# Performance work log

Measured on AMD Instinct MI355X. Metric: run time of the kernel, lower is better.

## Reference

```python
import jax, jax.numpy as jnp
import numpy as np

EPS = 1e-6  # AngularPhysicsConfig.eps


def setup_inputs() -> dict:
    key = jax.random.key(0)
    k1, k2 = jax.random.split(key)
    B, L, d, H = 2, 2048, 2048, 8
    x_spatial = jax.random.normal(k1, (B, L, d), dtype=jnp.float32)
    # attn is a softmax output: rows sum to 1 over the last axis
    attn = jax.nn.softmax(jax.random.normal(k2, (B, H, L, L), dtype=jnp.float32), axis=-1)
    W = jnp.ones((1,), dtype=jnp.float32)   # nn.Parameter(torch.ones(1))
    b = jnp.zeros((1,), dtype=jnp.float32)  # bias_init = 0.0
    return {"x_spatial": x_spatial, "attn": attn, "W": W, "b": b}


def reference(x_spatial, attn, W, b):
    # --- angular_kernel ---
    norm = jnp.clip(jnp.linalg.norm(x_spatial, axis=-1, keepdims=True), EPS, None)
    x_unit = x_spatial / norm                                   # [B, L, d]
    K = jnp.einsum('bld,bmd->blm', x_unit, x_unit)              # [B, L, L] cosine sim
    K_mean = K.mean(axis=(-1, -2), keepdims=True)
    K_cent = K - K_mean
    # torch .std() is unbiased (ddof=1), computed on detached K_cent
    K_std = jnp.std(jax.lax.stop_gradient(K_cent), axis=(-1, -2), keepdims=True, ddof=1)
    K_norm = K_cent / jnp.clip(K_std, EPS, None)                # [B, L, L]

    # --- compute_cos_align (detach_attn_for_alignment=True) ---
    A = jax.lax.stop_gradient(attn.mean(axis=1))                # [B, L, L]
    cos_align = jnp.sum(A * K_norm, axis=-1)                    # [B, L]

    # --- gate ---
    gate = jax.nn.sigmoid(W * cos_align + b)                    # [B, L]
    return gate, cos_align, K_norm
```

## Files before the change

### kernel.cpp

```cpp
#include <hip/hip_runtime.h>
#include <hip/hip_bf16.h>

#define L_DIM 2048
#define D_DIM 2048
#define B_DIM 2
#define H_DIM 8
#define NT 16
#define NPAIR 136
#define NRED 512
#define NKT (D_DIM / 64)
#define EPSV 1e-6f

using bf16x8 = __attribute__((ext_vector_type(8))) __bf16;
using f32x4  = __attribute__((ext_vector_type(4))) float;
using f4     = __attribute__((ext_vector_type(4))) float;

__device__ inline void gload_lds16(const void* g, void* l) {
    __builtin_amdgcn_global_load_lds(
        (const __attribute__((address_space(1))) void*)g,
        (__attribute__((address_space(3))) void*)l, 16, 0, 0);
}

__device__ inline ushort f2bf(float f) {
    unsigned int u = __float_as_uint(f);
    unsigned int lsb = (u >> 16) & 1u;
    u += 0x7fffu + lsb;
    return (ushort)(u >> 16);
}
__device__ inline float bf2f(ushort u) {
    return __uint_as_float(((unsigned int)u) << 16);
}

__global__ __launch_bounds__(256) void k_normalize(const float* __restrict__ x,
                                                   ushort* __restrict__ xu,
                                                   double* __restrict__ sums) {
    const int row = blockIdx.x;
    const int t   = threadIdx.x;
    const float* xr = x + (size_t)row * D_DIM;
    f4 v0 = __builtin_nontemporal_load(((const f4*)xr) + t);
    f4 v1 = __builtin_nontemporal_load(((const f4*)xr) + t + 256);
    float ss = v0.x*v0.x + v0.y*v0.y + v0.z*v0.z + v0.w*v0.w
             + v1.x*v1.x + v1.y*v1.y + v1.z*v1.z + v1.w*v1.w;
    #pragma unroll
    for (int off = 32; off; off >>= 1) ss += __shfl_down(ss, off);
    __shared__ float red[4];
    __shared__ float s_inv;
    if ((t & 63) == 0) red[t >> 6] = ss;
    __syncthreads();
    if (t == 0) {
        float nrm = sqrtf(red[0] + red[1] + red[2] + red[3]);
        nrm = fmaxf(nrm, EPSV);
        s_inv = 1.0f / nrm;
        if (row == 0) { sums[0] = 0.0; sums[1] = 0.0; sums[2] = 0.0; sums[3] = 0.0; }
    }
    __syncthreads();
    const float inv = s_inv;
    ushort* xo = xu + (size_t)row * D_DIM;
    ushort4 o0, o1;
    o0.x = f2bf(v0.x * inv); o0.y = f2bf(v0.y * inv);
    o0.z = f2bf(v0.z * inv); o0.w = f2bf(v0.w * inv);
    o1.x = f2bf(v1.x * inv); o1.y = f2bf(v1.y * inv);
    o1.z = f2bf(v1.z * inv); o1.w = f2bf(v1.w * inv);
    ((ushort4*)xo)[t]       = o0;
    ((ushort4*)xo)[t + 256] = o1;
}

__global__ __launch_bounds__(256) void k_mixed(const ushort* __restrict__ Xu,
                                               const float* __restrict__ attn,
                                               ushort* __restrict__ K16,
                                               double* __restrict__ sums,
                                               ushort* __restrict__ Amean) {
    __shared__ __align__(16) ushort lds_a[128 * 64];
    __shared__ __align__(16) ushort lds_b[128 * 64];
    const int t = threadIdx.x;
    const int batch = blockIdx.z;

    if (blockIdx.x >= NPAIR) {
        const int rid = blockIdx.x - NPAIR;
        const float* ab = attn + (size_t)batch * H_DIM * L_DIM * L_DIM;
        ushort* am = Amean + (size_t)batch * L_DIM * L_DIM;
        int i = rid * 256 + t;
        #pragma unroll
        for (int j = 0; j < 8; ++j, i += NRED * 256) {
            float4 s = {0.f, 0.f, 0.f, 0.f};
            #pragma unroll
            for (int h = 0; h < H_DIM; ++h) {
                const f4 v = __builtin_nontemporal_load(
                    ((const f4*)(ab + (size_t)h * L_DIM * L_DIM)) + i);
                s.x += v.x; s.y += v.y; s.z += v.z; s.w += v.w;
            }
            ushort4 o;
            o.x = f2bf(s.x * 0.125f); o.y = f2bf(s.y * 0.125f);
            o.z = f2bf(s.z * 0.125f); o.w = f2bf(s.w * 0.125f);
            ((ushort4*)am)[i] = o;
        }
        return;
    }

    const int lane = t & 63;
    const int w    = t >> 6;
    const int wr   = w >> 1, wc = w & 1;
    int ti = 0, rem = blockIdx.x;
    while (rem >= NT - ti) { rem -= NT - ti; ++ti; }
    const int tj = ti + rem;
    const int bRow = ti * 128;
    const int bCol = tj * 128;
    const bool diag = (ti == tj);
    const ushort* Xb = Xu + (size_t)batch * L_DIM * D_DIM;

    const int srow8  = t >> 3;
    const int schunk = ((t & 7) ^ (srow8 & 7)) * 8;
    const ushort* gA = Xb + (size_t)(bRow + srow8) * D_DIM + schunk;
    const ushort* gB = Xb + (size_t)(bCol + srow8) * D_DIM + schunk;
    ushort* lA = lds_a + t * 8;
    ushort* lB = lds_b + t * 8;

    f32x4 acc[4][4] = {};
    const int frow = lane & 15;
    const int fk   = lane >> 4;

    for (int kt = 0; kt < NKT; ++kt) {
        __syncthreads();
        const size_t ko = (size_t)kt * 64;
        #pragma unroll
        for (int i = 0; i < 4; ++i) {
            gload_lds16(gA + ko + (size_t)i * 32 * D_DIM, lA + i * 2048);
            gload_lds16(gB + ko + (size_t)i * 32 * D_DIM, lB + i * 2048);
        }
        __syncthreads();
        #pragma unroll
        for (int ks = 0; ks < 2; ++ks) {
            bf16x8 a[4], b[4];
            #pragma unroll
            for (int m = 0; m < 4; ++m) {
                const int R = wr * 64 + m * 16 + frow;
                a[m] = *(const bf16x8*)&lds_a[R * 64 + (((ks << 2) + fk) ^ (R & 7)) * 8];
            }
            #pragma unroll
            for (int n = 0; n < 4; ++n) {
                const int S = wc * 64 + n * 16 + frow;
                b[n] = *(const bf16x8*)&lds_b[S * 64 + (((ks << 2) + fk) ^ (S & 7)) * 8];
            }
            #pragma unroll
            for (int m = 0; m < 4; ++m)
                #pragma unroll
                for (int n = 0; n < 4; ++n)
                    acc[m][n] = __builtin_amdgcn_mfma_f32_16x16x32_bf16(a[m], b[n], acc[m][n], 0, 0, 0);
        }
    }

    ushort* Kb = K16 + (size_t)batch * L_DIM * L_DIM;
    float ps = 0.f, pss = 0.f;
    #pragma unroll
    for (int m = 0; m < 4; ++m) {
        #pragma unroll
        for (int n = 0; n < 4; ++n) {
            #pragma unroll
            for (int j = 0; j < 4; ++j) {
                const int r = bRow + wr * 64 + m * 16 + fk * 4 + j;
                const int c = bCol + wc * 64 + n * 16 + frow;
                const float v = acc[m][n][j];
                Kb[(size_t)r * L_DIM + c] = f2bf(v);
                ps += v; pss += v * v;
            }
            if (!diag) {
                const int rr  = bCol + wc * 64 + n * 16 + frow;
                const int cc0 = bRow + wr * 64 + m * 16 + fk * 4;
                ushort4 mq;
                mq.x = f2bf(acc[m][n][0]); mq.y = f2bf(acc[m][n][1]);
                mq.z = f2bf(acc[m][n][2]); mq.w = f2bf(acc[m][n][3]);
                *(ushort4*)&Kb[(size_t)rr * L_DIM + cc0] = mq;
            }
        }
    }
    if (!diag) { ps *= 2.f; pss *= 2.f; }
    #pragma unroll
    for (int off = 32; off; off >>= 1) {
        ps  += __shfl_down(ps, off);
        pss += __shfl_down(pss, off);
    }
    __shared__ float redS[4], redSS[4];
    if (lane == 0) { redS[w] = ps; redSS[w] = pss; }
    __syncthreads();
    if (t == 0) {
        atomicAdd(&sums[batch * 2],     (double)(redS[0] + redS[1] + redS[2] + redS[3]));
        atomicAdd(&sums[batch * 2 + 1], (double)(redSS[0] + redSS[1] + redSS[2] + redSS[3]));
    }
}

__global__ __launch_bounds__(256) void k_epilogue(float* __restrict__ out,
                                                  const ushort* __restrict__ K16,
                                                  const ushort* __restrict__ Amean,
                                                  const double* __restrict__ sums,
                                                  const float* __restrict__ Wp,
                                                  const float* __restrict__ bp) {
    const int row = blockIdx.x;
    const int b = row >> 11;
    const int t = threadIdx.x;

    const double N = (double)L_DIM * (double)L_DIM;
    const double mean_d = sums[b * 2] / N;
    double var = (sums[b * 2 + 1] - N * mean_d * mean_d) / (N - 1.0);
    var = var > 0.0 ? var : 0.0;
    float sd = (float)sqrt(var);
    sd = fmaxf(sd, EPSV);
    const float inv_std = 1.0f / sd;
    const float mean = (float)mean_d;

    const ushort* krow = K16 + (size_t)row * L_DIM;
    const ushort* arow = Amean + (size_t)row * L_DIM;
    float* onrm = out + 2 * B_DIM * L_DIM + (size_t)row * L_DIM;

    const ushort4 k0 = ((const ushort4*)krow)[t * 2];
    const ushort4 k1 = ((const ushort4*)krow)[t * 2 + 1];
    const ushort4 a0 = ((const ushort4*)arow)[t * 2];
    const ushort4 a1 = ((const ushort4*)arow)[t * 2 + 1];
    float kf[8] = { bf2f(k0.x), bf2f(k0.y), bf2f(k0.z), bf2f(k0.w),
                    bf2f(k1.x), bf2f(k1.y), bf2f(k1.z), bf2f(k1.w) };
    float af[8] = { bf2f(a0.x), bf2f(a0.y), bf2f(a0.z), bf2f(a0.w),
                    bf2f(a1.x), bf2f(a1.y), bf2f(a1.z), bf2f(a1.w) };
    float dot = 0.f;
    #pragma unroll
    for (int j = 0; j < 8; ++j) dot += af[j] * kf[j];
    f4 n0, n1;
    n0.x = (kf[0] - mean) * inv_std; n0.y = (kf[1] - mean) * inv_std;
    n0.z = (kf[2] - mean) * inv_std; n0.w = (kf[3] - mean) * inv_std;
    n1.x = (kf[4] - mean) * inv_std; n1.y = (kf[5] - mean) * inv_std;
    n1.z = (kf[6] - mean) * inv_std; n1.w = (kf[7] - mean) * inv_std;
    __builtin_nontemporal_store(n0, ((f4*)onrm) + t * 2);
    __builtin_nontemporal_store(n1, ((f4*)onrm) + t * 2 + 1);

    #pragma unroll
    for (int off = 32; off; off >>= 1) dot += __shfl_down(dot, off);
    __shared__ float red[4];
    if ((t & 63) == 0) red[t >> 6] = dot;
    __syncthreads();
    if (t == 0) {
        const float dotv = red[0] + red[1] + red[2] + red[3];
        const float ca = (dotv - mean) * inv_std;
        out[B_DIM * L_DIM + row] = ca;
        const float z = Wp[0] * ca + bp[0];
        out[row] = 1.0f / (1.0f + expf(-z));
    }
}

extern "C" void kernel_launch(void* const* d_in, const int* in_sizes, int n_in,
                              void* d_out, int out_size, void* d_ws, size_t ws_size,
                              hipStream_t stream) {
    const float* x    = (const float*)d_in[0];
    const float* attn = (const float*)d_in[1];
    const float* W    = (const float*)d_in[2];
    const float* bb   = (const float*)d_in[3];
    float* out = (float*)d_out;

    const size_t MAT = (size_t)B_DIM * L_DIM * L_DIM;
    ushort* xu    = (ushort*)d_ws;
    double* sums  = (double*)((char*)d_ws + MAT * 2);
    ushort* Amean = (ushort*)((char*)d_ws + MAT * 2 + 256);
    ushort* K16   = (ushort*)((char*)d_ws + MAT * 4 + 256);

    hipLaunchKernelGGL(k_normalize, dim3(B_DIM * L_DIM), dim3(256), 0, stream,
                       x, xu, sums);
    hipLaunchKernelGGL(k_mixed, dim3(NPAIR + NRED, 1, B_DIM), dim3(256), 0, stream,
                       xu, attn, K16, sums, Amean);
    hipLaunchKernelGGL(k_epilogue, dim3(B_DIM * L_DIM), dim3(256), 0, stream,
                       out, K16, Amean, sums, W, bb);
}
```

Measured before the change: 106.1 us.

## Fuse three kernels into one persistent cooperative kernel with grid syncs

Replaces the normalize, mixed GEMM/attn-mean, and epilogue kernels with a single cooperative persistent kernel of 512 blocks. Phase one normalizes rows and starts the attention head-mean. After a grid sync, 272 blocks run the Gram GEMM tiles while the remaining blocks finish the attention reduction. A second grid sync precedes the normalized-output epilogue. This removes two kernel launches and overlaps the GEMM with bandwidth-bound attention reads, at the cost of grid-sync overhead and fixed work partitioning with fewer blocks per phase.

```diff
diff --git a/kernel.cpp b/kernel.cpp
--- a/kernel.cpp
+++ b/kernel.cpp
@@ -1,5 +1,8 @@
 #include <hip/hip_runtime.h>
 #include <hip/hip_bf16.h>
+#include <hip/hip_cooperative_groups.h>
+
+namespace cg = cooperative_groups;
 
 #define L_DIM 2048
 #define D_DIM 2048
@@ -8,6 +11,10 @@
 #define NT 16
 #define NPAIR 136
 #define NRED 512
+#define NUNIT 8192
+#define P1U 6144
+#define NBLK 512
+#define ROWS_PB 8
 #define NKT (D_DIM / 64)
 #define EPSV 1e-6f
 
@@ -31,216 +38,239 @@
     return __uint_as_float(((unsigned int)u) << 16);
 }
 
-__global__ __launch_bounds__(256) void k_normalize(const float* __restrict__ x,
-                                                   ushort* __restrict__ xu,
-                                                   double* __restrict__ sums) {
-    const int row = blockIdx.x;
-    const int t   = threadIdx.x;
-    const float* xr = x + (size_t)row * D_DIM;
-    f4 v0 = __builtin_nontemporal_load(((const f4*)xr) + t);
-    f4 v1 = __builtin_nontemporal_load(((const f4*)xr) + t + 256);
-    float ss = v0.x*v0.x + v0.y*v0.y + v0.z*v0.z + v0.w*v0.w
-             + v1.x*v1.x + v1.y*v1.y + v1.z*v1.z + v1.w*v1.w;
+__device__ __forceinline__ void attn_unit(const float* __restrict__ attn,
+                                          ushort* __restrict__ Amean,
+                                          int u, int t) {
+    const int batch = u >> 12;
+    const int v     = u & 4095;
+    const int rid   = v & (NRED - 1);
+    const int j     = v >> 9;
+    const int i     = rid * 256 + j * (NRED * 256) + t;
+    const float* ab = attn + (size_t)batch * H_DIM * L_DIM * L_DIM;
+    float4 s = {0.f, 0.f, 0.f, 0.f};
     #pragma unroll
-    for (int off = 32; off; off >>= 1) ss += __shfl_down(ss, off);
-    __shared__ float red[4];
-    __shared__ float s_inv;
-    if ((t & 63) == 0) red[t >> 6] = ss;
-    __syncthreads();
-    if (t == 0) {
-        float nrm = sqrtf(red[0] + red[1] + red[2] + red[3]);
-        nrm = fmaxf(nrm, EPSV);
-        s_inv = 1.0f / nrm;
-        if (row == 0) { sums[0] = 0.0; sums[1] = 0.0; sums[2] = 0.0; sums[3] = 0.0; }
-    }
-    __syncthreads();
-    const float inv = s_inv;
-    ushort* xo = xu + (size_t)row * D_DIM;
-    ushort4 o0, o1;
-    o0.x = f2bf(v0.x * inv); o0.y = f2bf(v0.y * inv);
-    o0.z = f2bf(v0.z * inv); o0.w = f2bf(v0.w * inv);
-    o1.x = f2bf(v1.x * inv); o1.y = f2bf(v1.y * inv);
-    o1.z = f2bf(v1.z * inv); o1.w = f2bf(v1.w * inv);
-    ((ushort4*)xo)[t]       = o0;
-    ((ushort4*)xo)[t + 256] = o1;
-}
-
-__global__ __launch_bounds__(256) void k_mixed(const ushort* __restrict__ Xu,
-                                               const float* __restrict__ attn,
-                                               ushort* __restrict__ K16,
-                                               double* __restrict__ sums,
-                                               ushort* __restrict__ Amean) {
+    for (int h = 0; h < H_DIM; ++h) {
+        const f4 vv = __builtin_nontemporal_load(
+            ((const f4*)(ab + (size_t)h * L_DIM * L_DIM)) + i);
+        s.x += vv.x; s.y += vv.y; s.z += vv.z; s.w += vv.w;
+    }
+    ushort4 o;
+    o.x = f2bf(s.x * 0.125f); o.y = f2bf(s.y * 0.125f);
+    o.z = f2bf(s.z * 0.125f); o.w = f2bf(s.w * 0.125f);
+    ((ushort4*)(Amean + (size_t)batch * L_DIM * L_DIM))[i] = o;
+}
+
+__global__ __launch_bounds__(256, 2) void k_fused(const float* __restrict__ x,
+                                                  const float* __restrict__ attn,
+                                                  float* __restrict__ out,
+                                                  ushort* __restrict__ xu,
+                                                  ushort* __restrict__ K16,
+                                                  ushort* __restrict__ Amean,
+                                                  double* __restrict__ sums,
+                                                  const float* __restrict__ Wp,
+                                                  const float* __restrict__ bp) {
     __shared__ __align__(16) ushort lds_a[128 * 64];
     __shared__ __align__(16) ushort lds_b[128 * 64];
-    const int t = threadIdx.x;
-    const int batch = blockIdx.z;
-
-    if (blockIdx.x >= NPAIR) {
-        const int rid = blockIdx.x - NPAIR;
-        const float* ab = attn + (size_t)batch * H_DIM * L_DIM * L_DIM;
-        ushort* am = Amean + (size_t)batch * L_DIM * L_DIM;
-        int i = rid * 256 + t;
-        #pragma unroll
-        for (int j = 0; j < 8; ++j, i += NRED * 256) {
-            float4 s = {0.f, 0.f, 0.f, 0.f};
+    __shared__ float red[4];
+    __shared__ float sbc;
+    const int t   = threadIdx.x;
+    const int blk = blockIdx.x;
+    cg::grid_group grid = cg::this_grid();
+
+    if (blk == 0 && t < 4) sums[t] = 0.0;
+
+    for (int r = 0; r < ROWS_PB; ++r) {
+        const int row = blk * ROWS_PB + r;
+        const float* xr = x + (size_t)row * D_DIM;
+        f4 v0 = __builtin_nontemporal_load(((const f4*)xr) + t);
+        f4 v1 = __builtin_nontemporal_load(((const f4*)xr) + t + 256);
+        float ss = v0.x*v0.x + v0.y*v0.y + v0.z*v0.z + v0.w*v0.w
+                 + v1.x*v1.x + v1.y*v1.y + v1.z*v1.z + v1.w*v1.w;
+        #pragma unroll
+        for (int off = 32; off; off >>= 1) ss += __shfl_down(ss, off);
+        if ((t & 63) == 0) red[t >> 6] = ss;
+        __syncthreads();
+        if (t == 0) {
+            float nrm = sqrtf(red[0] + red[1] + red[2] + red[3]);
+            sbc = 1.0f / fmaxf(nrm, EPSV);
+        }
+        __syncthreads();
+        const float inv = sbc;
+        ushort* xo = xu + (size_t)row * D_DIM;
+        ushort4 o0, o1;
+        o0.x = f2bf(v0.x * inv); o0.y = f2bf(v0.y * inv);
+        o0.z = f2bf(v0.z * inv); o0.w = f2bf(v0.w * inv);
+        o1.x = f2bf(v1.x * inv); o1.y = f2bf(v1.y * inv);
+        o1.z = f2bf(v1.z * inv); o1.w = f2bf(v1.w * inv);
+        ((ushort4*)xo)[t]       = o0;
+        ((ushort4*)xo)[t + 256] = o1;
+        __syncthreads();
+    }
+    #pragma unroll 2
+    for (int k = 0; k < P1U / NBLK; ++k)
+        attn_unit(attn, Amean, blk * (P1U / NBLK) + k, t);
+
+    __threadfence();
+    grid.sync();
+
+    if (blk < 2 * NPAIR) {
+        const int lane = t & 63;
+        const int w    = t >> 6;
+        const int wr   = w >> 1, wc = w & 1;
+        const int batch = blk / NPAIR;
+        int ti = 0, rem = blk % NPAIR;
+        while (rem >= NT - ti) { rem -= NT - ti; ++ti; }
+        const int tj = ti + rem;
+        const int bRow = ti * 128;
+        const int bCol = tj * 128;
+        const bool diag = (ti == tj);
+        const ushort* Xb = xu + (size_t)batch * L_DIM * D_DIM;
+
+        const int srow8  = t >> 3;
+        const int schunk = ((t & 7) ^ (srow8 & 7)) * 8;
+        const ushort* gA = Xb + (size_t)(bRow + srow8) * D_DIM + schunk;
+        const ushort* gB = Xb + (size_t)(bCol + srow8) * D_DIM + schunk;
+        ushort* lA = lds_a + t * 8;
+        ushort* lB = lds_b + t * 8;
+
+        f32x4 acc[4][4] = {};
+        const int frow = lane & 15;
+        const int fk   = lane >> 4;
+
+        for (int kt = 0; kt < NKT; ++kt) {
+            __syncthreads();
+            const size_t ko = (size_t)kt * 64;
             #pragma unroll
-            for (int h = 0; h < H_DIM; ++h) {
-                const f4 v = __builtin_nontemporal_load(
-                    ((const f4*)(ab + (size_t)h * L_DIM * L_DIM)) + i);
-                s.x += v.x; s.y += v.y; s.z += v.z; s.w += v.w;
+            for (int i = 0; i < 4; ++i) {
+                gload_lds16(gA + ko + (size_t)i * 32 * D_DIM, lA + i * 2048);
+                gload_lds16(gB + ko + (size_t)i * 32 * D_DIM, lB + i * 2048);
             }
-            ushort4 o;
-            o.x = f2bf(s.x * 0.125f); o.y = f2bf(s.y * 0.125f);
-            o.z = f2bf(s.z * 0.125f); o.w = f2bf(s.w * 0.125f);
-            ((ushort4*)am)[i] = o;
-        }
-        return;
-    }
-
-    const int lane = t & 63;
-    const int w    = t >> 6;
-    const int wr   = w >> 1, wc = w & 1;
-    int ti = 0, rem = blockIdx.x;
-    while (rem >= NT - ti) { rem -= NT - ti; ++ti; }
-    const int tj = ti + rem;
-    const int bRow = ti * 128;
-    const int bCol = tj * 128;
-    const bool diag = (ti == tj);
-    const ushort* Xb = Xu + (size_t)batch * L_DIM * D_DIM;
-
-    const int srow8  = t >> 3;
-    const int schunk = ((t & 7) ^ (srow8 & 7)) * 8;
-    const ushort* gA = Xb + (size_t)(bRow + srow8) * D_DIM + schunk;
-    const ushort* gB = Xb + (size_t)(bCol + srow8) * D_DIM + schunk;
-    ushort* lA = lds_a + t * 8;
-    ushort* lB = lds_b + t * 8;
-
-    f32x4 acc[4][4] = {};
-    const int frow = lane & 15;
-    const int fk   = lane >> 4;
-
-    for (int kt = 0; kt < NKT; ++kt) {
-        __syncthreads();
-        const size_t ko = (size_t)kt * 64;
-        #pragma unroll
-        for (int i = 0; i < 4; ++i) {
-            gload_lds16(gA + ko + (size_t)i * 32 * D_DIM, lA + i * 2048);
-            gload_lds16(gB + ko + (size_t)i * 32 * D_DIM, lB + i * 2048);
-        }
-        __syncthreads();
-        #pragma unroll
-        for (int ks = 0; ks < 2; ++ks) {
-            bf16x8 a[4], b[4];
+            __syncthreads();
             #pragma unroll
-            for (int m = 0; m < 4; ++m) {
-                const int R = wr * 64 + m * 16 + frow;
-                a[m] = *(const bf16x8*)&lds_a[R * 64 + (((ks << 2) + fk) ^ (R & 7)) * 8];
+            for (int ks = 0; ks < 2; ++ks) {
+                bf16x8 a[4], b[4];
+                #pragma unroll
+                for (int m = 0; m < 4; ++m) {
+                    const int R = wr * 64 + m * 16 + frow;
+                    a[m] = *(const bf16x8*)&lds_a[R * 64 + (((ks << 2) + fk) ^ (R & 7)) * 8];
+                }
+                #pragma unroll
+                for (int n = 0; n < 4; ++n) {
+                    const int S = wc * 64 + n * 16 + frow;
+                    b[n] = *(const bf16x8*)&lds_b[S * 64 + (((ks << 2) + fk) ^ (S & 7)) * 8];
+                }
+                #pragma unroll
+                for (int m = 0; m < 4; ++m)
+                    #pragma unroll
+                    for (int n = 0; n < 4; ++n)
+                        acc[m][n] = __builtin_amdgcn_mfma_f32_16x16x32_bf16(a[m], b[n], acc[m][n], 0, 0, 0);
             }
+        }
+
+        ushort* Kb = K16 + (size_t)batch * L_DIM * L_DIM;
+        float ps = 0.f, pss = 0.f;
+        #pragma unroll
+        for (int m = 0; m < 4; ++m) {
             #pragma unroll
             for (int n = 0; n < 4; ++n) {
-                const int S = wc * 64 + n * 16 + frow;
-                b[n] = *(const bf16x8*)&lds_b[S * 64 + (((ks << 2) + fk) ^ (S & 7)) * 8];
+                #pragma unroll
+                for (int j = 0; j < 4; ++j) {
+                    const int r = bRow + wr * 64 + m * 16 + fk * 4 + j;
+                    const int c = bCol + wc * 64 + n * 16 + frow;
+                    const float v = acc[m][n][j];
+                    Kb[(size_t)r * L_DIM + c] = f2bf(v);
+                    ps += v; pss += v * v;
+                }
+                if (!diag) {
+                    const int rr  = bCol + wc * 64 + n * 16 + frow;
+                    const int cc0 = bRow + wr * 64 + m * 16 + fk * 4;
+                    ushort4 mq;
+                    mq.x = f2bf(acc[m][n][0]); mq.y = f2bf(acc[m][n][1]);
+                    mq.z = f2bf(acc[m][n][2]); mq.w = f2bf(acc[m][n][3]);
+                    *(ushort4*)&Kb[(size_t)rr * L_DIM + cc0] = mq;
+                }
             }
-            #pragma unroll
-            for (int m = 0; m < 4; ++m)
-                #pragma unroll
-                for (int n = 0; n < 4; ++n)
-                    acc[m][n] = __builtin_amdgcn_mfma_f32_16x16x32_bf16(a[m], b[n], acc[m][n], 0, 0, 0);
-        }
-    }
-
-    ushort* Kb = K16 + (size_t)batch * L_DIM * L_DIM;
-    float ps = 0.f, pss = 0.f;
+        }
+        if (!diag) { ps *= 2.f; pss *= 2.f; }
+        #pragma unroll
+        for (int off = 32; off; off >>= 1) {
+            ps  += __shfl_down(ps, off);
+            pss += __shfl_down(pss, off);
+        }
+        __syncthreads();
+        if (lane == 0) red[w] = ps;
+        __syncthreads();
+        const float psum = red[0] + red[1] + red[2] + red[3];
+        __syncthreads();
+        if (lane == 0) red[w] = pss;
+        __syncthreads();
+        if (t == 0) {
+            atomicAdd(&sums[batch * 2],     (double)psum);
+            atomicAdd(&sums[batch * 2 + 1], (double)(red[0] + red[1] + red[2] + red[3]));
+        }
+    } else {
+        const int i0 = blk - 2 * NPAIR;
+        #pragma unroll 2
+        for (int k = 0; k < 9; ++k) {
+            const int u = P1U + i0 + 240 * k;
+            if (u < NUNIT) attn_unit(attn, Amean, u, t);
+        }
+    }
+
+    __threadfence();
+    grid.sync();
+
+    const double N = (double)L_DIM * (double)L_DIM;
+    float mean_b[2], inv_b[2];
     #pragma unroll
-    for (int m = 0; m < 4; ++m) {
-        #pragma unroll
-        for (int n = 0; n < 4; ++n) {
-            #pragma unroll
-            for (int j = 0; j < 4; ++j) {
-                const int r = bRow + wr * 64 + m * 16 + fk * 4 + j;
-                const int c = bCol + wc * 64 + n * 16 + frow;
-                const float v = acc[m][n][j];
-                Kb[(size_t)r * L_DIM + c] = f2bf(v);
-                ps += v; pss += v * v;
-            }
-            if (!diag) {
-                const int rr  = bCol + wc * 64 + n * 16 + frow;
-                const int cc0 = bRow + wr * 64 + m * 16 + fk * 4;
-                ushort4 mq;
-                mq.x = f2bf(acc[m][n][0]); mq.y = f2bf(acc[m][n][1]);
-                mq.z = f2bf(acc[m][n][2]); mq.w = f2bf(acc[m][n][3]);
-                *(ushort4*)&Kb[(size_t)rr * L_DIM + cc0] = mq;
-            }
-        }
-    }
-    if (!diag) { ps *= 2.f; pss *= 2.f; }
-    #pragma unroll
-    for (int off = 32; off; off >>= 1) {
-        ps  += __shfl_down(ps, off);
-        pss += __shfl_down(pss, off);
-    }
-    __shared__ float redS[4], redSS[4];
-    if (lane == 0) { redS[w] = ps; redSS[w] = pss; }
-    __syncthreads();
-    if (t == 0) {
-        atomicAdd(&sums[batch * 2],     (double)(redS[0] + redS[1] + redS[2] + redS[3]));
-        atomicAdd(&sums[batch * 2 + 1], (double)(redSS[0] + redSS[1] + redSS[2] + redSS[3]));
-    }
-}
-
-__global__ __launch_bounds__(256) void k_epilogue(float* __restrict__ out,
-                                                  const ushort* __restrict__ K16,
-                                                  const ushort* __restrict__ Amean,
-                                                  const double* __restrict__ sums,
-                                                  const float* __restrict__ Wp,
-                                                  const float* __restrict__ bp) {
-    const int row = blockIdx.x;
-    const int b = row >> 11;
-    const int t = threadIdx.x;
-
-    const double N = (double)L_DIM * (double)L_DIM;
-    const double mean_d = sums[b * 2] / N;
-    double var = (sums[b * 2 + 1] - N * mean_d * mean_d) / (N - 1.0);
-    var = var > 0.0 ? var : 0.0;
-    float sd = (float)sqrt(var);
-    sd = fmaxf(sd, EPSV);
-    const float inv_std = 1.0f / sd;
-    const float mean = (float)mean_d;
-
-    const ushort* krow = K16 + (size_t)row * L_DIM;
-    const ushort* arow = Amean + (size_t)row * L_DIM;
-    float* onrm = out + 2 * B_DIM * L_DIM + (size_t)row * L_DIM;
-
-    const ushort4 k0 = ((const ushort4*)krow)[t * 2];
-    const ushort4 k1 = ((const ushort4*)krow)[t * 2 + 1];
-    const ushort4 a0 = ((const ushort4*)arow)[t * 2];
-    const ushort4 a1 = ((const ushort4*)arow)[t * 2 + 1];
-    float kf[8] = { bf2f(k0.x), bf2f(k0.y), bf2f(k0.z), bf2f(k0.w),
-                    bf2f(k1.x), bf2f(k1.y), bf2f(k1.z), bf2f(k1.w) };
-    float af[8] = { bf2f(a0.x), bf2f(a0.y), bf2f(a0.z), bf2f(a0.w),
-                    bf2f(a1.x), bf2f(a1.y), bf2f(a1.z), bf2f(a1.w) };
-    float dot = 0.f;
-    #pragma unroll
-    for (int j = 0; j < 8; ++j) dot += af[j] * kf[j];
-    f4 n0, n1;
-    n0.x = (kf[0] - mean) * inv_std; n0.y = (kf[1] - mean) * inv_std;
-    n0.z = (kf[2] - mean) * inv_std; n0.w = (kf[3] - mean) * inv_std;
-    n1.x = (kf[4] - mean) * inv_std; n1.y = (kf[5] - mean) * inv_std;
-    n1.z = (kf[6] - mean) * inv_std; n1.w = (kf[7] - mean) * inv_std;
-    __builtin_nontemporal_store(n0, ((f4*)onrm) + t * 2);
-    __builtin_nontemporal_store(n1, ((f4*)onrm) + t * 2 + 1);
-
-    #pragma unroll
-    for (int off = 32; off; off >>= 1) dot += __shfl_down(dot, off);
-    __shared__ float red[4];
-    if ((t & 63) == 0) red[t >> 6] = dot;
-    __syncthreads();
-    if (t == 0) {
-        const float dotv = red[0] + red[1] + red[2] + red[3];
-        const float ca = (dotv - mean) * inv_std;
-        out[B_DIM * L_DIM + row] = ca;
-        const float z = Wp[0] * ca + bp[0];
-        out[row] = 1.0f / (1.0f + expf(-z));
+    for (int bb = 0; bb < 2; ++bb) {
+        const double mean_d = sums[bb * 2] / N;
+        double var = (sums[bb * 2 + 1] - N * mean_d * mean_d) / (N - 1.0);
+        var = var > 0.0 ? var : 0.0;
+        float sd = fmaxf((float)sqrt(var), EPSV);
+        mean_b[bb] = (float)mean_d;
+        inv_b[bb]  = 1.0f / sd;
+    }
+    const float Wv = Wp[0], bv = bp[0];
+
+    for (int r = 0; r < ROWS_PB; ++r) {
+        const int row = blk * ROWS_PB + r;
+        const int b = row >> 11;
+        const float mean = mean_b[b], inv_std = inv_b[b];
+        const ushort* krow = K16 + (size_t)row * L_DIM;
+        const ushort* arow = Amean + (size_t)row * L_DIM;
+        float* onrm = out + 2 * B_DIM * L_DIM + (size_t)row * L_DIM;
+
+        const ushort4 k0 = ((const ushort4*)krow)[t * 2];
+        const ushort4 k1 = ((const ushort4*)krow)[t * 2 + 1];
+        const ushort4 a0 = ((const ushort4*)arow)[t * 2];
+        const ushort4 a1 = ((const ushort4*)arow)[t * 2 + 1];
+        float kf[8] = { bf2f(k0.x), bf2f(k0.y), bf2f(k0.z), bf2f(k0.w),
+                        bf2f(k1.x), bf2f(k1.y), bf2f(k1.z), bf2f(k1.w) };
+        float af[8] = { bf2f(a0.x), bf2f(a0.y), bf2f(a0.z), bf2f(a0.w),
+                        bf2f(a1.x), bf2f(a1.y), bf2f(a1.z), bf2f(a1.w) };
+        float dot = 0.f;
+        #pragma unroll
+        for (int j = 0; j < 8; ++j) dot += af[j] * kf[j];
+        f4 n0, n1;
+        n0.x = (kf[0] - mean) * inv_std; n0.y = (kf[1] - mean) * inv_std;
+        n0.z = (kf[2] - mean) * inv_std; n0.w = (kf[3] - mean) * inv_std;
+        n1.x = (kf[4] - mean) * inv_std; n1.y = (kf[5] - mean) * inv_std;
+        n1.z = (kf[6] - mean) * inv_std; n1.w = (kf[7] - mean) * inv_std;
+        __builtin_nontemporal_store(n0, ((f4*)onrm) + t * 2);
+        __builtin_nontemporal_store(n1, ((f4*)onrm) + t * 2 + 1);
+
+        #pragma unroll
+        for (int off = 32; off; off >>= 1) dot += __shfl_down(dot, off);
+        if ((t & 63) == 0) red[t >> 6] = dot;
+        __syncthreads();
+        if (t == 0) {
+            const float dotv = red[0] + red[1] + red[2] + red[3];
+            const float ca = (dotv - mean) * inv_std;
+            out[B_DIM * L_DIM + row] = ca;
+            out[row] = 1.0f / (1.0f + expf(-(Wv * ca + bv)));
+        }
+        __syncthreads();
     }
 }
 
@@ -259,10 +289,7 @@
     ushort* Amean = (ushort*)((char*)d_ws + MAT * 2 + 256);
     ushort* K16   = (ushort*)((char*)d_ws + MAT * 4 + 256);
 
-    hipLaunchKernelGGL(k_normalize, dim3(B_DIM * L_DIM), dim3(256), 0, stream,
-                       x, xu, sums);
-    hipLaunchKernelGGL(k_mixed, dim3(NPAIR + NRED, 1, B_DIM), dim3(256), 0, stream,
-                       xu, attn, K16, sums, Amean);
-    hipLaunchKernelGGL(k_epilogue, dim3(B_DIM * L_DIM), dim3(256), 0, stream,
-                       out, K16, Amean, sums, W, bb);
-}
+    void* args[] = { (void*)&x, (void*)&attn, (void*)&out, (void*)&xu,
+                     (void*)&K16, (void*)&Amean, (void*)&sums, (void*)&W, (void*)&bb };
+    hipLaunchCooperativeKernel((void*)k_fused, dim3(NBLK), dim3(256), args, 0, stream);
+}
```

Result: slower. 403.3 us (+280.1%).

## Dynamically schedule attention-mean work via atomic counter across all blocks

Applied to the files above, without the earlier changes.

Replaces the static split, where dedicated blocks each reduced eight fixed attention chunks, with a work queue driven by a global atomic counter. Every block, including the GEMM tile blocks once their tile is done, pulls pairs of attention-mean units until the 8192 units are consumed. This is meant to balance the memory-bound head reduction against the compute-bound Gram tiles so neither side leaves CUs idle. It adds atomic contention, two extra barriers per grab, and a counter reset in the normalize kernel.

```diff
diff --git a/kernel.cpp b/kernel.cpp
--- a/kernel.cpp
+++ b/kernel.cpp
@@ -8,6 +8,8 @@
 #define NT 16
 #define NPAIR 136
 #define NRED 512
+#define NUNIT 8192
+#define NSTREAM 512
 #define NKT (D_DIM / 64)
 #define EPSV 1e-6f
 
@@ -31,9 +33,32 @@
     return __uint_as_float(((unsigned int)u) << 16);
 }
 
+__device__ __forceinline__ void attn_unit(const float* __restrict__ attn,
+                                          ushort* __restrict__ Amean,
+                                          int u, int t) {
+    const int batch = u >> 12;
+    const int v     = u & 4095;
+    const int rid   = v & (NRED - 1);
+    const int j     = v >> 9;
+    const int i     = rid * 256 + j * (NRED * 256) + t;
+    const float* ab = attn + (size_t)batch * H_DIM * L_DIM * L_DIM;
+    float4 s = {0.f, 0.f, 0.f, 0.f};
+    #pragma unroll
+    for (int h = 0; h < H_DIM; ++h) {
+        const f4 vv = __builtin_nontemporal_load(
+            ((const f4*)(ab + (size_t)h * L_DIM * L_DIM)) + i);
+        s.x += vv.x; s.y += vv.y; s.z += vv.z; s.w += vv.w;
+    }
+    ushort4 o;
+    o.x = f2bf(s.x * 0.125f); o.y = f2bf(s.y * 0.125f);
+    o.z = f2bf(s.z * 0.125f); o.w = f2bf(s.w * 0.125f);
+    ((ushort4*)(Amean + (size_t)batch * L_DIM * L_DIM))[i] = o;
+}
+
 __global__ __launch_bounds__(256) void k_normalize(const float* __restrict__ x,
                                                    ushort* __restrict__ xu,
-                                                   double* __restrict__ sums) {
+                                                   double* __restrict__ sums,
+                                                   unsigned int* __restrict__ ctr) {
     const int row = blockIdx.x;
     const int t   = threadIdx.x;
     const float* xr = x + (size_t)row * D_DIM;
@@ -51,7 +76,10 @@
         float nrm = sqrtf(red[0] + red[1] + red[2] + red[3]);
         nrm = fmaxf(nrm, EPSV);
         s_inv = 1.0f / nrm;
-        if (row == 0) { sums[0] = 0.0; sums[1] = 0.0; sums[2] = 0.0; sums[3] = 0.0; }
+        if (row == 0) {
+            sums[0] = 0.0; sums[1] = 0.0; sums[2] = 0.0; sums[3] = 0.0;
+            ctr[0] = 0u;
+        }
     }
     __syncthreads();
     const float inv = s_inv;
@@ -69,122 +97,114 @@
                                                const float* __restrict__ attn,
                                                ushort* __restrict__ K16,
                                                double* __restrict__ sums,
-                                               ushort* __restrict__ Amean) {
+                                               ushort* __restrict__ Amean,
+                                               unsigned int* __restrict__ ctr) {
     __shared__ __align__(16) ushort lds_a[128 * 64];
     __shared__ __align__(16) ushort lds_b[128 * 64];
+    __shared__ unsigned int su;
     const int t = threadIdx.x;
     const int batch = blockIdx.z;
 
-    if (blockIdx.x >= NPAIR) {
-        const int rid = blockIdx.x - NPAIR;
-        const float* ab = attn + (size_t)batch * H_DIM * L_DIM * L_DIM;
-        ushort* am = Amean + (size_t)batch * L_DIM * L_DIM;
-        int i = rid * 256 + t;
+    if (blockIdx.x < NPAIR) {
+        const int lane = t & 63;
+        const int w    = t >> 6;
+        const int wr   = w >> 1, wc = w & 1;
+        int ti = 0, rem = blockIdx.x;
+        while (rem >= NT - ti) { rem -= NT - ti; ++ti; }
+        const int tj = ti + rem;
+        const int bRow = ti * 128;
+        const int bCol = tj * 128;
+        const bool diag = (ti == tj);
+        const ushort* Xb = Xu + (size_t)batch * L_DIM * D_DIM;
+
+        const int srow8  = t >> 3;
+        const int schunk = ((t & 7) ^ (srow8 & 7)) * 8;
+        const ushort* gA = Xb + (size_t)(bRow + srow8) * D_DIM + schunk;
+        const ushort* gB = Xb + (size_t)(bCol + srow8) * D_DIM + schunk;
+        ushort* lA = lds_a + t * 8;
+        ushort* lB = lds_b + t * 8;
+
+        f32x4 acc[4][4] = {};
+        const int frow = lane & 15;
+        const int fk   = lane >> 4;
+
+        for (int kt = 0; kt < NKT; ++kt) {
+            __syncthreads();
+            const size_t ko = (size_t)kt * 64;
+            #pragma unroll
+            for (int i = 0; i < 4; ++i) {
+                gload_lds16(gA + ko + (size_t)i * 32 * D_DIM, lA + i * 2048);
+                gload_lds16(gB + ko + (size_t)i * 32 * D_DIM, lB + i * 2048);
+            }
+            __syncthreads();
+            #pragma unroll
+            for (int ks = 0; ks < 2; ++ks) {
+                bf16x8 a[4], b[4];
+                #pragma unroll
+                for (int m = 0; m < 4; ++m) {
+                    const int R = wr * 64 + m * 16 + frow;
+                    a[m] = *(const bf16x8*)&lds_a[R * 64 + (((ks << 2) + fk) ^ (R & 7)) * 8];
+                }
+                #pragma unroll
+                for (int n = 0; n < 4; ++n) {
+                    const int S = wc * 64 + n * 16 + frow;
+                    b[n] = *(const bf16x8*)&lds_b[S * 64 + (((ks << 2) + fk) ^ (S & 7)) * 8];
+                }
+                #pragma unroll
+                for (int m = 0; m < 4; ++m)
+                    #pragma unroll
+                    for (int n = 0; n < 4; ++n)
+                        acc[m][n] = __builtin_amdgcn_mfma_f32_16x16x32_bf16(a[m], b[n], acc[m][n], 0, 0, 0);
+            }
+        }
+
+        ushort* Kb = K16 + (size_t)batch * L_DIM * L_DIM;
+        float ps = 0.f, pss = 0.f;
         #pragma unroll
-        for (int j = 0; j < 8; ++j, i += NRED * 256) {
-            float4 s = {0.f, 0.f, 0.f, 0.f};
-            #pragma unroll
-            for (int h = 0; h < H_DIM; ++h) {
-                const f4 v = __builtin_nontemporal_load(
-                    ((const f4*)(ab + (size_t)h * L_DIM * L_DIM)) + i);
-                s.x += v.x; s.y += v.y; s.z += v.z; s.w += v.w;
-            }
-            ushort4 o;
-            o.x = f2bf(s.x * 0.125f); o.y = f2bf(s.y * 0.125f);
-            o.z = f2bf(s.z * 0.125f); o.w = f2bf(s.w * 0.125f);
-            ((ushort4*)am)[i] = o;
-        }
-        return;
-    }
-
-    const int lane = t & 63;
-    const int w    = t >> 6;
-    const int wr   = w >> 1, wc = w & 1;
-    int ti = 0, rem = blockIdx.x;
-    while (rem >= NT - ti) { rem -= NT - ti; ++ti; }
-    const int tj = ti + rem;
-    const int bRow = ti * 128;
-    const int bCol = tj * 128;
-    const bool diag = (ti == tj);
-    const ushort* Xb = Xu + (size_t)batch * L_DIM * D_DIM;
-
-    const int srow8  = t >> 3;
-    const int schunk = ((t & 7) ^ (srow8 & 7)) * 8;
-    const ushort* gA = Xb + (size_t)(bRow + srow8) * D_DIM + schunk;
-    const ushort* gB = Xb + (size_t)(bCol + srow8) * D_DIM + schunk;
-    ushort* lA = lds_a + t * 8;
-    ushort* lB = lds_b + t * 8;
-
-    f32x4 acc[4][4] = {};
-    const int frow = lane & 15;
-    const int fk   = lane >> 4;
-
-    for (int kt = 0; kt < NKT; ++kt) {
-        __syncthreads();
-        const size_t ko = (size_t)kt * 64;
-        #pragma unroll
-        for (int i = 0; i < 4; ++i) {
-            gload_lds16(gA + ko + (size_t)i * 32 * D_DIM, lA + i * 2048);
-            gload_lds16(gB + ko + (size_t)i * 32 * D_DIM, lB + i * 2048);
-        }
-        __syncthreads();
-        #pragma unroll
-        for (int ks = 0; ks < 2; ++ks) {
-            bf16x8 a[4], b[4];
-            #pragma unroll
-            for (int m = 0; m < 4; ++m) {
-                const int R = wr * 64 + m * 16 + frow;
-                a[m] = *(const bf16x8*)&lds_a[R * 64 + (((ks << 2) + fk) ^ (R & 7)) * 8];
-            }
+        for (int m = 0; m < 4; ++m) {
             #pragma unroll
             for (int n = 0; n < 4; ++n) {
-                const int S = wc * 64 + n * 16 + frow;
-                b[n] = *(const bf16x8*)&lds_b[S * 64 + (((ks << 2) + fk) ^ (S & 7)) * 8];
+                #pragma unroll
+                for (int j = 0; j < 4; ++j) {
+                    const int r = bRow + wr * 64 + m * 16 + fk * 4 + j;
+                    const int c = bCol + wc * 64 + n * 16 + frow;
+                    const float v = acc[m][n][j];
+                    Kb[(size_t)r * L_DIM + c] = f2bf(v);
+                    ps += v; pss += v * v;
+                }
+                if (!diag) {
+                    const int rr  = bCol + wc * 64 + n * 16 + frow;
+                    const int cc0 = bRow + wr * 64 + m * 16 + fk * 4;
+                    ushort4 mq;
+                    mq.x = f2bf(acc[m][n][0]); mq.y = f2bf(acc[m][n][1]);
+                    mq.z = f2bf(acc[m][n][2]); mq.w = f2bf(acc[m][n][3]);
+                    *(ushort4*)&Kb[(size_t)rr * L_DIM + cc0] = mq;
+                }
             }
-            #pragma unroll
-            for (int m = 0; m < 4; ++m)
-                #pragma unroll
-                for (int n = 0; n < 4; ++n)
-                    acc[m][n] = __builtin_amdgcn_mfma_f32_16x16x32_bf16(a[m], b[n], acc[m][n], 0, 0, 0);
-        }
-    }
-
-    ushort* Kb = K16 + (size_t)batch * L_DIM * L_DIM;
-    float ps = 0.f, pss = 0.f;
-    #pragma unroll
-    for (int m = 0; m < 4; ++m) {
+        }
+        if (!diag) { ps *= 2.f; pss *= 2.f; }
         #pragma unroll
-        for (int n = 0; n < 4; ++n) {
-            #pragma unroll
-            for (int j = 0; j < 4; ++j) {
-                const int r = bRow + wr * 64 + m * 16 + fk * 4 + j;
-                const int c = bCol + wc * 64 + n * 16 + frow;
-                const float v = acc[m][n][j];
-                Kb[(size_t)r * L_DIM + c] = f2bf(v);
-                ps += v; pss += v * v;
-            }
-            if (!diag) {
-                const int rr  = bCol + wc * 64 + n * 16 + frow;
-                const int cc0 = bRow + wr * 64 + m * 16 + fk * 4;
-                ushort4 mq;
-                mq.x = f2bf(acc[m][n][0]); mq.y = f2bf(acc[m][n][1]);
-                mq.z = f2bf(acc[m][n][2]); mq.w = f2bf(acc[m][n][3]);
-                *(ushort4*)&Kb[(size_t)rr * L_DIM + cc0] = mq;
-            }
-        }
-    }
-    if (!diag) { ps *= 2.f; pss *= 2.f; }
-    #pragma unroll
-    for (int off = 32; off; off >>= 1) {
-        ps  += __shfl_down(ps, off);
-        pss += __shfl_down(pss, off);
-    }
-    __shared__ float redS[4], redSS[4];
-    if (lane == 0) { redS[w] = ps; redSS[w] = pss; }
-    __syncthreads();
-    if (t == 0) {
-        atomicAdd(&sums[batch * 2],     (double)(redS[0] + redS[1] + redS[2] + redS[3]));
-        atomicAdd(&sums[batch * 2 + 1], (double)(redSS[0] + redSS[1] + redSS[2] + redSS[3]));
+        for (int off = 32; off; off >>= 1) {
+            ps  += __shfl_down(ps, off);
+            pss += __shfl_down(pss, off);
+        }
+        __shared__ float redS[4], redSS[4];
+        if (lane == 0) { redS[w] = ps; redSS[w] = pss; }
+        __syncthreads();
+        if (t == 0) {
+            atomicAdd(&sums[batch * 2],     (double)(redS[0] + redS[1] + redS[2] + redS[3]));
+            atomicAdd(&sums[batch * 2 + 1], (double)(redSS[0] + redSS[1] + redSS[2] + redSS[3]));
+        }
+    }
+
+    for (;;) {
+        if (t == 0) su = atomicAdd(ctr, 2u);
+        __syncthreads();
+        const unsigned int u = su;
+        __syncthreads();
+        if (u >= NUNIT) break;
+        attn_unit(attn, Amean, (int)u, t);
+        if (u + 1 < NUNIT) attn_unit(attn, Amean, (int)(u + 1), t);
     }
 }
 
@@ -256,13 +276,14 @@
     const size_t MAT = (size_t)B_DIM * L_DIM * L_DIM;
     ushort* xu    = (ushort*)d_ws;
     double* sums  = (double*)((char*)d_ws + MAT * 2);
+    unsigned int* ctr = (unsigned int*)((char*)d_ws + MAT * 2 + 64);
     ushort* Amean = (ushort*)((char*)d_ws + MAT * 2 + 256);
     ushort* K16   = (ushort*)((char*)d_ws + MAT * 4 + 256);
 
     hipLaunchKernelGGL(k_normalize, dim3(B_DIM * L_DIM), dim3(256), 0, stream,
-                       x, xu, sums);
-    hipLaunchKernelGGL(k_mixed, dim3(NPAIR + NRED, 1, B_DIM), dim3(256), 0, stream,
-                       xu, attn, K16, sums, Amean);
+                       x, xu, sums, ctr);
+    hipLaunchKernelGGL(k_mixed, dim3(NPAIR + NSTREAM, 1, B_DIM), dim3(256), 0, stream,
+                       xu, attn, K16, sums, Amean, ctr);
     hipLaunchKernelGGL(k_epilogue, dim3(B_DIM * L_DIM), dim3(256), 0, stream,
                        out, K16, Amean, sums, W, bb);
 }
```

Result: slower. 141.1 us (+33.0%).

## Fuse normalize into mixed kernel with flag-based producer/consumer sync

Applied to the files above, without the earlier changes.

Folds the row-normalization kernel into the mixed kernel. Normalize blocks process 8 rows each, then signal per-tile flags with release atomics, and GEMM blocks spin-wait on the flags for their two row tiles. Normalize blocks then take a share of the attention-mean streaming work, and the remaining attention blocks run unconditionally. This removes one kernel launch boundary and lets the bandwidth-bound attention reduction overlap with normalization and GEMM, at the cost of a memset, spin-waiting that depends on block scheduling order, and a risk of deadlock if GEMM blocks occupy the slots the normalize blocks need.

```diff
diff --git a/kernel.cpp b/kernel.cpp
--- a/kernel.cpp
+++ b/kernel.cpp
@@ -8,6 +8,9 @@
 #define NT 16
 #define NPAIR 136
 #define NRED 512
+#define NNORM 512
+#define NSTR 768
+#define NGEMM (2 * NPAIR)
 #define NKT (D_DIM / 64)
 #define EPSV 1e-6f
 
@@ -31,82 +34,111 @@
     return __uint_as_float(((unsigned int)u) << 16);
 }
 
-__global__ __launch_bounds__(256) void k_normalize(const float* __restrict__ x,
-                                                   ushort* __restrict__ xu,
-                                                   double* __restrict__ sums) {
-    const int row = blockIdx.x;
-    const int t   = threadIdx.x;
-    const float* xr = x + (size_t)row * D_DIM;
-    f4 v0 = __builtin_nontemporal_load(((const f4*)xr) + t);
-    f4 v1 = __builtin_nontemporal_load(((const f4*)xr) + t + 256);
-    float ss = v0.x*v0.x + v0.y*v0.y + v0.z*v0.z + v0.w*v0.w
-             + v1.x*v1.x + v1.y*v1.y + v1.z*v1.z + v1.w*v1.w;
-    #pragma unroll
-    for (int off = 32; off; off >>= 1) ss += __shfl_down(ss, off);
+__device__ __forceinline__ void attn_unit(const float* __restrict__ attn,
+                                          ushort* __restrict__ Amean,
+                                          int job, int j, int t) {
+    const int batch = job >> 9;
+    const int rid   = job & (NRED - 1);
+    const int i     = rid * 256 + j * (NRED * 256) + t;
+    const float* ab = attn + (size_t)batch * H_DIM * L_DIM * L_DIM;
+    float4 s = {0.f, 0.f, 0.f, 0.f};
+    #pragma unroll
+    for (int h = 0; h < H_DIM; ++h) {
+        const f4 vv = __builtin_nontemporal_load(
+            ((const f4*)(ab + (size_t)h * L_DIM * L_DIM)) + i);
+        s.x += vv.x; s.y += vv.y; s.z += vv.z; s.w += vv.w;
+    }
+    ushort4 o;
+    o.x = f2bf(s.x * 0.125f); o.y = f2bf(s.y * 0.125f);
+    o.z = f2bf(s.z * 0.125f); o.w = f2bf(s.w * 0.125f);
+    ((ushort4*)(Amean + (size_t)batch * L_DIM * L_DIM))[i] = o;
+}
+
+__global__ __launch_bounds__(256) void k_mixed(const float* __restrict__ x,
+                                               const float* __restrict__ attn,
+                                               ushort* __restrict__ xu,
+                                               ushort* __restrict__ K16,
+                                               double* __restrict__ sums,
+                                               ushort* __restrict__ Amean,
+                                               unsigned int* __restrict__ flags) {
+    __shared__ __align__(16) ushort lds_a[128 * 64];
+    __shared__ __align__(16) ushort lds_b[128 * 64];
     __shared__ float red[4];
     __shared__ float s_inv;
-    if ((t & 63) == 0) red[t >> 6] = ss;
-    __syncthreads();
-    if (t == 0) {
-        float nrm = sqrtf(red[0] + red[1] + red[2] + red[3]);
-        nrm = fmaxf(nrm, EPSV);
-        s_inv = 1.0f / nrm;
-        if (row == 0) { sums[0] = 0.0; sums[1] = 0.0; sums[2] = 0.0; sums[3] = 0.0; }
-    }
-    __syncthreads();
-    const float inv = s_inv;
-    ushort* xo = xu + (size_t)row * D_DIM;
-    ushort4 o0, o1;
-    o0.x = f2bf(v0.x * inv); o0.y = f2bf(v0.y * inv);
-    o0.z = f2bf(v0.z * inv); o0.w = f2bf(v0.w * inv);
-    o1.x = f2bf(v1.x * inv); o1.y = f2bf(v1.y * inv);
-    o1.z = f2bf(v1.z * inv); o1.w = f2bf(v1.w * inv);
-    ((ushort4*)xo)[t]       = o0;
-    ((ushort4*)xo)[t + 256] = o1;
-}
-
-__global__ __launch_bounds__(256) void k_mixed(const ushort* __restrict__ Xu,
-                                               const float* __restrict__ attn,
-                                               ushort* __restrict__ K16,
-                                               double* __restrict__ sums,
-                                               ushort* __restrict__ Amean) {
-    __shared__ __align__(16) ushort lds_a[128 * 64];
-    __shared__ __align__(16) ushort lds_b[128 * 64];
-    const int t = threadIdx.x;
-    const int batch = blockIdx.z;
-
-    if (blockIdx.x >= NPAIR) {
-        const int rid = blockIdx.x - NPAIR;
-        const float* ab = attn + (size_t)batch * H_DIM * L_DIM * L_DIM;
-        ushort* am = Amean + (size_t)batch * L_DIM * L_DIM;
-        int i = rid * 256 + t;
-        #pragma unroll
-        for (int j = 0; j < 8; ++j, i += NRED * 256) {
-            float4 s = {0.f, 0.f, 0.f, 0.f};
-            #pragma unroll
-            for (int h = 0; h < H_DIM; ++h) {
-                const f4 v = __builtin_nontemporal_load(
-                    ((const f4*)(ab + (size_t)h * L_DIM * L_DIM)) + i);
-                s.x += v.x; s.y += v.y; s.z += v.z; s.w += v.w;
-            }
-            ushort4 o;
-            o.x = f2bf(s.x * 0.125f); o.y = f2bf(s.y * 0.125f);
-            o.z = f2bf(s.z * 0.125f); o.w = f2bf(s.w * 0.125f);
-            ((ushort4*)am)[i] = o;
-        }
+    const int t   = threadIdx.x;
+    const int bid = blockIdx.x;
+
+    if (bid < NNORM) {
+        for (int r = 0; r < 8; ++r) {
+            const int row = bid * 8 + r;
+            const float* xr = x + (size_t)row * D_DIM;
+            f4 v0 = __builtin_nontemporal_load(((const f4*)xr) + t);
+            f4 v1 = __builtin_nontemporal_load(((const f4*)xr) + t + 256);
+            float ss = v0.x*v0.x + v0.y*v0.y + v0.z*v0.z + v0.w*v0.w
+                     + v1.x*v1.x + v1.y*v1.y + v1.z*v1.z + v1.w*v1.w;
+            #pragma unroll
+            for (int off = 32; off; off >>= 1) ss += __shfl_down(ss, off);
+            if ((t & 63) == 0) red[t >> 6] = ss;
+            __syncthreads();
+            if (t == 0) {
+                float nrm = sqrtf(red[0] + red[1] + red[2] + red[3]);
+                s_inv = 1.0f / fmaxf(nrm, EPSV);
+            }
+            __syncthreads();
+            const float inv = s_inv;
+            ushort* xo = xu + (size_t)row * D_DIM;
+            ushort4 o0, o1;
+            o0.x = f2bf(v0.x * inv); o0.y = f2bf(v0.y * inv);
+            o0.z = f2bf(v0.z * inv); o0.w = f2bf(v0.w * inv);
+            o1.x = f2bf(v1.x * inv); o1.y = f2bf(v1.y * inv);
+            o1.z = f2bf(v1.z * inv); o1.w = f2bf(v1.w * inv);
+            ((ushort4*)xo)[t]       = o0;
+            ((ushort4*)xo)[t + 256] = o1;
+            __syncthreads();
+        }
+        if (t == 0) {
+            __threadfence();
+            __hip_atomic_fetch_add(&flags[bid >> 4], 1u,
+                                   __ATOMIC_RELEASE, __HIP_MEMORY_SCOPE_AGENT);
+        }
+        if (bid == 0 && t < 4) sums[t] = 0.0;
+        const int job = NSTR + (bid >> 1);
+        const int j0  = (bid & 1) * 4;
+        #pragma unroll
+        for (int k = 0; k < 4; ++k)
+            attn_unit(attn, Amean, job, j0 + k, t);
         return;
     }
 
-    const int lane = t & 63;
-    const int w    = t >> 6;
-    const int wr   = w >> 1, wc = w & 1;
-    int ti = 0, rem = blockIdx.x;
+    if (bid < NNORM + NSTR) {
+        const int job = bid - NNORM;
+        #pragma unroll
+        for (int j = 0; j < 8; ++j)
+            attn_unit(attn, Amean, job, j, t);
+        return;
+    }
+
+    const int idx   = bid - NNORM - NSTR;
+    const int batch = idx >= NPAIR ? 1 : 0;
+    int ti = 0, rem = idx - batch * NPAIR;
     while (rem >= NT - ti) { rem -= NT - ti; ++ti; }
     const int tj = ti + rem;
     const int bRow = ti * 128;
     const int bCol = tj * 128;
     const bool diag = (ti == tj);
-    const ushort* Xb = Xu + (size_t)batch * L_DIM * D_DIM;
+
+    if (t == 0) {
+        const int fa = batch * 16 + ti, fb = batch * 16 + tj;
+        while (__hip_atomic_load(&flags[fa], __ATOMIC_ACQUIRE, __HIP_MEMORY_SCOPE_AGENT) < 16u ||
+               __hip_atomic_load(&flags[fb], __ATOMIC_ACQUIRE, __HIP_MEMORY_SCOPE_AGENT) < 16u)
+            __builtin_amdgcn_s_sleep(8);
+    }
+    __syncthreads();
+
+    const int lane = t & 63;
+    const int w    = t >> 6;
+    const int wr   = w >> 1, wc = w & 1;
+    const ushort* Xb = xu + (size_t)batch * L_DIM * D_DIM;
 
     const int srow8  = t >> 3;
     const int schunk = ((t & 7) ^ (srow8 & 7)) * 8;
@@ -256,13 +288,14 @@
     const size_t MAT = (size_t)B_DIM * L_DIM * L_DIM;
     ushort* xu    = (ushort*)d_ws;
     double* sums  = (double*)((char*)d_ws + MAT * 2);
+    unsigned int* flags = (unsigned int*)((char*)d_ws + MAT * 2 + 64);
     ushort* Amean = (ushort*)((char*)d_ws + MAT * 2 + 256);
     ushort* K16   = (ushort*)((char*)d_ws + MAT * 4 + 256);
 
-    hipLaunchKernelGGL(k_normalize, dim3(B_DIM * L_DIM), dim3(256), 0, stream,
-                       x, xu, sums);
-    hipLaunchKernelGGL(k_mixed, dim3(NPAIR + NRED, 1, B_DIM), dim3(256), 0, stream,
-                       xu, attn, K16, sums, Amean);
+    hipMemsetAsync((char*)d_ws + MAT * 2, 0, 256, stream);
+
+    hipLaunchKernelGGL(k_mixed, dim3(NNORM + NSTR + NGEMM), dim3(256), 0, stream,
+                       x, attn, xu, K16, sums, Amean, flags);
     hipLaunchKernelGGL(k_epilogue, dim3(B_DIM * L_DIM), dim3(256), 0, stream,
                        out, K16, Amean, sums, W, bb);
 }
```

Result: slower. 171.0 us (+61.2%).
